# Performance work log

Measured on AMD Instinct MI355X. Metric: run time of the kernel, lower is better.

## Reference

```python
import jax, jax.numpy as jnp
import numpy as np

EPS = 1e-8  # torch F.cosine_similarity default eps


def setup_inputs() -> dict:
    key = jax.random.key(0)
    k1, k2 = jax.random.split(key)
    x = jax.random.normal(k1, (16384, 1024), dtype=jnp.float32)
    label = jax.random.randint(k2, (16384, 64), 0, 2).astype(jnp.int64)
    w = jnp.asarray(10.0, dtype=jnp.float32)  # nn.Parameter init_w
    b = jnp.asarray(-5.0, dtype=jnp.float32)  # nn.Parameter init_b
    return {"x": x, "label": label, "w": w, "b": b}


def reference(x, label, w, b):
    # Append the 'no-label' column for rows whose label vector is all zero.
    extra = (label.sum(axis=1) == 0).astype(label.dtype)[:, None]
    lab = jnp.concatenate([label, extra], axis=1).astype(x.dtype)  # [B, C]

    counts = lab.sum(axis=0)                  # [C] positives per centroid
    active = counts > 0                       # torch drops empty columns; we mask them

    # Centroids: mean of x over rows carrying each label (scatter-mean as GEMM).
    anchor = (lab.T @ x) / jnp.maximum(counts, 1.0)[:, None]   # [C, D]

    # Cosine similarity between every sample and every centroid.
    xn = jnp.maximum(jnp.linalg.norm(x, axis=1), EPS)          # [B]
    an = jnp.maximum(jnp.linalg.norm(anchor, axis=1), EPS)     # [C]
    cos = (x @ anchor.T) / (xn[:, None] * an[None, :])          # [B, C]

    logits = cos * w + b
    # Removing empty columns from softmax == setting their logits to -inf.
    logits = jnp.where(active[None, :], logits, -jnp.inf)
    logp = jax.nn.log_softmax(logits, axis=1)                   # [B, C]

    # Row expansion in torch duplicates sample i once per positive label j;
    # the logits row only depends on i, so CE over expanded rows is a
    # pair-weighted mean of -logp[i, j] over positive (i, j) pairs.
    n_pairs = lab.sum()
    nloss = -jnp.sum(jnp.where(lab > 0, logp, 0.0)) / n_pairs
    return nloss
```

## Files before the change

kernel.cpp:

```cpp
#include <hip/hip_runtime.h>
#include <hip/hip_bf16.h>
#include <stdint.h>

#define NROWS 16384
#define NDIM  1024
#define NLAB  64
#define NC    65
#define CPAD  80

typedef float float4v __attribute__((ext_vector_type(4)));
typedef short short8  __attribute__((ext_vector_type(8)));

static constexpr size_t SCALE_B = 0;
static constexpr size_t ACTB_B  = 320;
static constexpr size_t WSUM_B  = 400;
static constexpr size_t CNTF_B  = 448;
static constexpr size_t CNTP_B  = 1024;
static constexpr size_t MASK_B  = 83968;
static constexpr size_t XN2_B   = 215040;
static constexpr size_t LFRAG_B = 280576;
static constexpr size_t BFRAG_B = 2902016;
static constexpr size_t XAF_B   = 3065856;
static constexpr size_t XCOL_B  = 36620288;
static constexpr size_t PART_B  = 70174720;
static constexpr size_t SLAB    = (size_t)CPAD * NDIM * 4;

__device__ __forceinline__ unsigned short bf16u(float f) {
    __hip_bfloat16 h = __float2bfloat16(f);
    return __builtin_bit_cast(unsigned short, h);
}
__device__ __forceinline__ unsigned pk2(float a, float b) {
    return (unsigned)bf16u(a) | ((unsigned)bf16u(b) << 16);
}

__global__ __launch_bounds__(256) void k01_prep(const float* __restrict__ x,
                                                const int* __restrict__ label,
                                                unsigned short* __restrict__ xAfrag,
                                                unsigned short* __restrict__ xcol,
                                                float* __restrict__ xn2g,
                                                unsigned long long* __restrict__ masks,
                                                unsigned* __restrict__ cntpart,
                                                unsigned short* __restrict__ lfrag) {
    __shared__ unsigned short xt[16][1034];
    __shared__ unsigned cnt[NC];
    __shared__ unsigned long long smask[64];
    int t = threadIdx.x;
    if (blockIdx.x < 1024) {
        int rt = blockIdx.x;
        int r = t >> 4, cpos = t & 15;
        const float* src = x + ((size_t)rt * 16 + r) * NDIM + cpos * 4;
        float sq = 0.f;
#pragma unroll
        for (int i = 0; i < 16; ++i) {
            float4 f = *(const float4*)(src + i * 64);
            sq += f.x * f.x + f.y * f.y + f.z * f.z + f.w * f.w;
            *(uint2*)&xt[r][cpos * 4 + i * 64] = make_uint2(pk2(f.x, f.y), pk2(f.z, f.w));
        }
#pragma unroll
        for (int m = 1; m < 16; m <<= 1) sq += __shfl_xor(sq, m, 16);
        if (cpos == 0) xn2g[rt * 16 + r] = sq;
        __syncthreads();
        {
            int slot = t & 63, wv = t >> 6;
            int q = slot >> 4, col = slot & 15;
#pragma unroll
            for (int s = 0; s < 8; ++s) {
                int kb = s * 4 + wv;
                uint4 v = *(const uint4*)&xt[col][kb * 32 + q * 8];
                ((uint4*)xAfrag)[((size_t)rt * 32 + kb) * 64 + slot] = v;
            }
        }
#pragma unroll
        for (int s = 0; s < 8; ++s) {
            int dim = s * 128 + (t >> 1);
            int rh = (t & 1) * 8;
            unsigned short tmp[8];
#pragma unroll
            for (int j = 0; j < 8; ++j) tmp[j] = xt[rh + j][dim];
            uint4 v;
            v.x = (unsigned)tmp[0] | ((unsigned)tmp[1] << 16);
            v.y = (unsigned)tmp[2] | ((unsigned)tmp[3] << 16);
            v.z = (unsigned)tmp[4] | ((unsigned)tmp[5] << 16);
            v.w = (unsigned)tmp[6] | ((unsigned)tmp[7] << 16);
            ((uint4*)xcol)[(size_t)rt * 2048 + s * 256 + t] = v;
        }
        return;
    }
    int bid = blockIdx.x - 1024;
    if (t < NC) cnt[t] = 0;
    __syncthreads();
    int wave = t >> 6, lane = t & 63;
    int rowblock = bid * 64;
    unsigned creg = 0, zreg = 0;
#pragma unroll 4
    for (int p = 0; p < 16; ++p) {
        int row = rowblock + p * 4 + wave;
        int v = label[row * NLAB + lane];
        unsigned long long m = __ballot(v != 0);
        creg += (unsigned)((m >> lane) & 1ull);
        if (lane == 0) {
            masks[row] = m;
            smask[p * 4 + wave] = m;
            zreg += (m == 0ull) ? 1u : 0u;
        }
    }
    atomicAdd(&cnt[lane], creg);
    if (lane == 0 && zreg) atomicAdd(&cnt[64], zreg);
    __syncthreads();
    if (t < 80) cntpart[bid * 80 + t] = (t < NC) ? cnt[t] : 0u;
    for (int pid = t; pid < 640; pid += 256) {
        int rt2l = pid / 320, rem = pid % 320;
        int ct = rem >> 6, ln = rem & 63;
        int q = ln >> 4, col = ln & 15;
        int c = ct * 16 + col;
        int rbase = rt2l * 32 + q * 8;
        unsigned pk[4];
#pragma unroll
        for (int jp = 0; jp < 4; ++jp) {
            unsigned long long m0 = smask[rbase + jp * 2], m1 = smask[rbase + jp * 2 + 1];
            unsigned b0, b1;
            if (c < 64)       { b0 = (unsigned)((m0 >> c) & 1ull); b1 = (unsigned)((m1 >> c) & 1ull); }
            else if (c == 64) { b0 = (m0 == 0ull); b1 = (m1 == 0ull); }
            else              { b0 = 0u; b1 = 0u; }
            pk[jp] = (b0 ? 0x3F80u : 0u) | (b1 ? 0x3F800000u : 0u);
        }
        uint4 w = make_uint4(pk[0], pk[1], pk[2], pk[3]);
        ((uint4*)lfrag)[((size_t)(bid * 2 + rt2l) * 5 + ct) * 64 + ln] = w;
    }
}

__global__ __launch_bounds__(256) void k2_sums(const unsigned short* __restrict__ xcol,
                                               const unsigned short* __restrict__ lfrag,
                                               float* __restrict__ partial,
                                               int kslices) {
    int t = threadIdx.x, wave = t >> 6, lane = t & 63;
    int q = lane >> 4, col = lane & 15;
    int dgroup = blockIdx.x & 15, ks = blockIdx.x >> 4;
    int nkb = (NROWS / kslices) >> 5;
    int kb0 = ks * nkb;
    int d = dgroup * 64 + wave * 16 + col;
    const uint4* B = (const uint4*)xcol;
    const uint4* A = (const uint4*)lfrag;
    size_t bidx0 = (size_t)d * 2 + (q & 1);
    int qh = q >> 1;

    float4v acc[5];
#pragma unroll
    for (int ct = 0; ct < 5; ++ct) acc[ct] = (float4v){0.f, 0.f, 0.f, 0.f};

    uint4 b0 = B[(size_t)((kb0 + 0) * 2 + qh) * 2048 + bidx0];
    uint4 a0[5];
#pragma unroll
    for (int ct = 0; ct < 5; ++ct) a0[ct] = A[((size_t)(kb0 + 0) * 5 + ct) * 64 + lane];
    uint4 b1 = B[(size_t)((kb0 + 1) * 2 + qh) * 2048 + bidx0];
    uint4 a1[5];
#pragma unroll
    for (int ct = 0; ct < 5; ++ct) a1[ct] = A[((size_t)(kb0 + 1) * 5 + ct) * 64 + lane];

    for (int i = 0; i < nkb; i += 2) {
        int p2 = i + 2 < nkb ? kb0 + i + 2 : kb0 + i;
        int p3 = i + 3 < nkb ? kb0 + i + 3 : kb0 + i + 1;
        {
            short8 bf = __builtin_bit_cast(short8, b0);
#pragma unroll
            for (int ct = 0; ct < 5; ++ct) {
                short8 af = __builtin_bit_cast(short8, a0[ct]);
                acc[ct] = __builtin_amdgcn_mfma_f32_16x16x32_bf16(af, bf, acc[ct], 0, 0, 0);
            }
            b0 = B[(size_t)(p2 * 2 + qh) * 2048 + bidx0];
#pragma unroll
            for (int ct = 0; ct < 5; ++ct) a0[ct] = A[((size_t)p2 * 5 + ct) * 64 + lane];
        }
        {
            short8 bf = __builtin_bit_cast(short8, b1);
#pragma unroll
            for (int ct = 0; ct < 5; ++ct) {
                short8 af = __builtin_bit_cast(short8, a1[ct]);
                acc[ct] = __builtin_amdgcn_mfma_f32_16x16x32_bf16(af, bf, acc[ct], 0, 0, 0);
            }
            b1 = B[(size_t)(p3 * 2 + qh) * 2048 + bidx0];
#pragma unroll
            for (int ct = 0; ct < 5; ++ct) a1[ct] = A[((size_t)p3 * 5 + ct) * 64 + lane];
        }
    }
    float* pb = partial + (size_t)ks * CPAD * NDIM;
#pragma unroll
    for (int ct = 0; ct < 5; ++ct)
#pragma unroll
        for (int reg = 0; reg < 4; ++reg)
            pb[(size_t)(ct * 16 + q * 4 + reg) * NDIM + d] = acc[ct][reg];
}

__global__ __launch_bounds__(1024) void k2b_fuse(const float* __restrict__ wptr,
                                                 const unsigned* __restrict__ cntpart,
                                                 const float* __restrict__ partial,
                                                 int kslices,
                                                 unsigned short* __restrict__ bfrag,
                                                 float* __restrict__ scale,
                                                 unsigned char* __restrict__ actB,
                                                 unsigned* __restrict__ countsF,
                                                 float* __restrict__ wsum) {
    int c = blockIdx.x, t = threadIdx.x;
    __shared__ float red[16];
    __shared__ unsigned credu[4];
    __shared__ float bcast[2];
    if (c == 0 && t == 512) *wsum = 0.f;
    if (t < 256) {
        unsigned cv = cntpart[t * 80 + c];
#pragma unroll
        for (int m = 32; m >= 1; m >>= 1) cv += __shfl_xor(cv, m, 64);
        if ((t & 63) == 0) credu[t >> 6] = cv;
    }
    __syncthreads();
    unsigned cnt = credu[0] + credu[1] + credu[2] + credu[3];

    const float* p = partial + (size_t)c * NDIM + t;
    float s = 0.f;
#pragma unroll 8
    for (int sl = 0; sl < kslices; ++sl)
        s += p[(size_t)sl * CPAD * NDIM];
    float invc = 1.0f / (float)(cnt > 0u ? cnt : 1u);
    float a = s * invc;
    float ss = a * a;
#pragma unroll
    for (int m = 32; m >= 1; m >>= 1) ss += __shfl_xor(ss, m, 64);
    if ((t & 63) == 0) red[t >> 6] = ss;
    __syncthreads();
    if (t == 0) {
        float tot = 0.f;
#pragma unroll
        for (int j = 0; j < 16; ++j) tot += red[j];
        bcast[0] = fmaxf(sqrtf(tot), 1e-8f);
    }
    __syncthreads();
    float rinv = 1.0f / bcast[0];
    unsigned short h = bf16u(a * rinv);
    int ct = c >> 4, colc = c & 15;
    int kb = t >> 5, q = (t >> 3) & 3, j0 = t & 7;
    bfrag[((((size_t)ct * 32 + kb) * 64) + q * 16 + colc) * 8 + j0] = h;
    float hv = __bfloat162float(__builtin_bit_cast(__hip_bfloat16, h));
    float nb2 = hv * hv;
#pragma unroll
    for (int m = 32; m >= 1; m >>= 1) nb2 += __shfl_xor(nb2, m, 64);
    if ((t & 63) == 0) red[t >> 6] = nb2;
    __syncthreads();
    if (t == 0) {
        float n2 = 0.f;
#pragma unroll
        for (int j = 0; j < 16; ++j) n2 += red[j];
        scale[c] = (n2 > 0.f) ? (wptr[0] / sqrtf(n2)) : 0.f;
        actB[c] = (cnt > 0u) ? 1 : 0;
        countsF[c] = cnt;
    }
}

__global__ __launch_bounds__(256) void k3_loss(const unsigned short* __restrict__ xAfrag,
                                               const unsigned short* __restrict__ bfrag,
                                               const float* __restrict__ xn2g,
                                               const unsigned long long* __restrict__ masks,
                                               const unsigned char* __restrict__ actB,
                                               const float* __restrict__ scale,
                                               const float* __restrict__ bptr,
                                               float* __restrict__ wsum) {
    int t = threadIdx.x, wave = t >> 6, lane = t & 63;
    int q = lane >> 4, col = lane & 15;
    int rt = blockIdx.x * 4 + wave;
    int rowbase = rt * 16;
    const uint4* A = (const uint4*)xAfrag + (size_t)rt * 32 * 64 + lane;
    const uint4* Bp = (const uint4*)bfrag + lane;

    float4v acc[5];
#pragma unroll
    for (int ct = 0; ct < 5; ++ct) acc[ct] = (float4v){0.f, 0.f, 0.f, 0.f};

    uint4 a0 = A[0], a1 = A[64];
    uint4 b0[5], b1[5];
#pragma unroll
    for (int ct = 0; ct < 5; ++ct) b0[ct] = Bp[(size_t)(ct * 32 + 0) * 64];
#pragma unroll
    for (int ct = 0; ct < 5; ++ct) b1[ct] = Bp[(size_t)(ct * 32 + 1) * 64];

    for (int s = 0; s < 32; s += 2) {
        int p2 = s + 2 < 32 ? s + 2 : s;
        int p3 = s + 3 < 32 ? s + 3 : s + 1;
        {
            short8 af = __builtin_bit_cast(short8, a0);
#pragma unroll
            for (int ct = 0; ct < 5; ++ct) {
                short8 bf = __builtin_bit_cast(short8, b0[ct]);
                acc[ct] = __builtin_amdgcn_mfma_f32_16x16x32_bf16(af, bf, acc[ct], 0, 0, 0);
            }
            a0 = A[p2 * 64];
#pragma unroll
            for (int ct = 0; ct < 5; ++ct) b0[ct] = Bp[(size_t)(ct * 32 + p2) * 64];
        }
        {
            short8 af = __builtin_bit_cast(short8, a1);
#pragma unroll
            for (int ct = 0; ct < 5; ++ct) {
                short8 bf = __builtin_bit_cast(short8, b1[ct]);
                acc[ct] = __builtin_amdgcn_mfma_f32_16x16x32_bf16(af, bf, acc[ct], 0, 0, 0);
            }
            a1 = A[p3 * 64];
#pragma unroll
            for (int ct = 0; ct < 5; ++ct) b1[ct] = Bp[(size_t)(ct * 32 + p3) * 64];
        }
    }

    float bv = bptr[0];
    float sc[5]; unsigned char ab[5];
#pragma unroll
    for (int ct = 0; ct < 5; ++ct) { sc[ct] = scale[ct * 16 + col]; ab[ct] = actB[ct * 16 + col]; }

    float contrib = 0.f;
#pragma unroll
    for (int reg = 0; reg < 4; ++reg) {
        int rl = q * 4 + reg;
        int row = rowbase + rl;
        float inv = 1.0f / fmaxf(sqrtf(xn2g[row]), 1e-8f);
        unsigned long long mask = masks[row];
        float v[5]; float lmax = -1e30f;
#pragma unroll
        for (int ct = 0; ct < 5; ++ct) {
            float lg = acc[ct][reg] * sc[ct] * inv + bv;
            v[ct] = ab[ct] ? lg : -1e30f;
            lmax = fmaxf(lmax, v[ct]);
        }
#pragma unroll
        for (int m = 1; m < 16; m <<= 1) lmax = fmaxf(lmax, __shfl_xor(lmax, m, 16));
        float es = 0.f;
#pragma unroll
        for (int ct = 0; ct < 5; ++ct) es += expf(v[ct] - lmax);
#pragma unroll
        for (int m = 1; m < 16; m <<= 1) es += __shfl_xor(es, m, 16);
        float lse = lmax + logf(es);
        float ps = 0.f;
#pragma unroll
        for (int ct = 0; ct < 5; ++ct) {
            int c = ct * 16 + col;
            bool pos = (c < 64) ? (((mask >> c) & 1ull) != 0ull)
                                : ((c == 64) ? (mask == 0ull) : false);
            ps += pos ? v[ct] : 0.f;
        }
#pragma unroll
        for (int m = 1; m < 16; m <<= 1) ps += __shfl_xor(ps, m, 16);
        float npos = mask ? (float)__popcll(mask) : 1.0f;
        float crow = ps - npos * lse;
        if (col == 0) contrib += crow;
    }
#pragma unroll
    for (int m = 1; m < 64; m <<= 1) contrib += __shfl_xor(contrib, m, 64);
    if (lane == 0) atomicAdd(wsum, contrib);
}

__global__ void k4_final(const unsigned* __restrict__ countsF,
                         const float* __restrict__ wsum,
                         float* __restrict__ out) {
    if (threadIdx.x == 0 && blockIdx.x == 0) {
        float np = 0.f;
        for (int c = 0; c < NC; ++c) np += (float)countsF[c];
        out[0] = -wsum[0] / np;
    }
}

extern "C" void kernel_launch(void* const* d_in, const int* in_sizes, int n_in,
                              void* d_out, int out_size, void* d_ws, size_t ws_size,
                              hipStream_t stream) {
    (void)in_sizes; (void)n_in; (void)out_size;
    const float* x = (const float*)d_in[0];
    const int* label = (const int*)d_in[1];
    const float* w = (const float*)d_in[2];
    const float* b = (const float*)d_in[3];

    char* ws = (char*)d_ws;
    float* scale = (float*)(ws + SCALE_B);
    unsigned char* actB = (unsigned char*)(ws + ACTB_B);
    float* wsum = (float*)(ws + WSUM_B);
    unsigned* countsF = (unsigned*)(ws + CNTF_B);
    unsigned* cntpart = (unsigned*)(ws + CNTP_B);
    unsigned long long* masks = (unsigned long long*)(ws + MASK_B);
    float* xn2g = (float*)(ws + XN2_B);
    unsigned short* lfrag = (unsigned short*)(ws + LFRAG_B);
    unsigned short* bfrag = (unsigned short*)(ws + BFRAG_B);
    unsigned short* xAfrag = (unsigned short*)(ws + XAF_B);
    unsigned short* xcol = (unsigned short*)(ws + XCOL_B);
    float* partial = (float*)(ws + PART_B);

    int kslices = 32;
    while (kslices > 8 && PART_B + (size_t)kslices * SLAB > ws_size) kslices >>= 1;

    hipLaunchKernelGGL(k01_prep, dim3(1024 + 256), dim3(256), 0, stream,
                       x, label, xAfrag, xcol, xn2g, masks, cntpart, lfrag);
    hipLaunchKernelGGL(k2_sums, dim3(16 * kslices), dim3(256), 0, stream,
                       xcol, lfrag, partial, kslices);
    hipLaunchKernelGGL(k2b_fuse, dim3(CPAD), dim3(1024), 0, stream,
                       w, cntpart, partial, kslices, bfrag, scale, actB, countsF, wsum);
    hipLaunchKernelGGL(k3_loss, dim3(NROWS / 64), dim3(256), 0, stream,
                       xAfrag, bfrag, xn2g, masks, actB, scale, b, wsum);
    hipLaunchKernelGGL(k4_final, dim3(1), dim3(64), 0, stream, countsF, wsum, (float*)d_out);
}
```

Measured before the change: 163.3 us.

## Restructure prep transpose, split centroid reduction, and split-K the loss GEMM

In the prep kernel, all x loads are issued before any use, and the xcol transpose now reads shared memory as 128-bit vectors and interleaves them with byte-permute into a new xcol layout. The k2_sums indexing is updated to match that layout. The centroid reduction is split into a wide kernel over 320 blocks that sums the k-slices and partial norms, plus a small finalize kernel, and k-slices go from 32 to 64. The loss GEMM now assigns one 16-row tile per block with split-K across its four waves, reduced through shared memory. These changes aim to add parallelism and memory-level concurrency, at the cost of one extra launch, more partial traffic and shared-memory reductions.

```diff
diff --git a/kernel.cpp b/kernel.cpp
--- a/kernel.cpp
+++ b/kernel.cpp
@@ -24,6 +24,8 @@
 static constexpr size_t XCOL_B  = 36620288;
 static constexpr size_t PART_B  = 70174720;
 static constexpr size_t SLAB    = (size_t)CPAD * NDIM * 4;
+static constexpr size_t ANCH_SZ = (size_t)CPAD * NDIM * 4;
+static constexpr size_t NRM_SZ  = (size_t)CPAD * 4 * 4;
 
 __device__ __forceinline__ unsigned short bf16u(float f) {
     __hip_bfloat16 h = __float2bfloat16(f);
@@ -41,20 +43,22 @@
                                                 unsigned long long* __restrict__ masks,
                                                 unsigned* __restrict__ cntpart,
                                                 unsigned short* __restrict__ lfrag) {
-    __shared__ unsigned short xt[16][1034];
+    __shared__ unsigned short xt[16][1040];
     __shared__ unsigned cnt[NC];
     __shared__ unsigned long long smask[64];
     int t = threadIdx.x;
     if (blockIdx.x < 1024) {
         int rt = blockIdx.x;
         int r = t >> 4, cpos = t & 15;
-        const float* src = x + ((size_t)rt * 16 + r) * NDIM + cpos * 4;
+        const float4* src = (const float4*)(x + ((size_t)rt * 16 + r) * NDIM) + cpos;
+        float4 f[16];
+#pragma unroll
+        for (int i = 0; i < 16; ++i) f[i] = src[i * 16];
         float sq = 0.f;
 #pragma unroll
         for (int i = 0; i < 16; ++i) {
-            float4 f = *(const float4*)(src + i * 64);
-            sq += f.x * f.x + f.y * f.y + f.z * f.z + f.w * f.w;
-            *(uint2*)&xt[r][cpos * 4 + i * 64] = make_uint2(pk2(f.x, f.y), pk2(f.z, f.w));
+            sq += f[i].x * f[i].x + f[i].y * f[i].y + f[i].z * f[i].z + f[i].w * f[i].w;
+            *(uint2*)&xt[r][cpos * 4 + i * 64] = make_uint2(pk2(f[i].x, f[i].y), pk2(f[i].z, f[i].w));
         }
 #pragma unroll
         for (int m = 1; m < 16; m <<= 1) sq += __shfl_xor(sq, m, 16);
@@ -70,19 +74,25 @@
                 ((uint4*)xAfrag)[((size_t)rt * 32 + kb) * 64 + slot] = v;
             }
         }
-#pragma unroll
-        for (int s = 0; s < 8; ++s) {
-            int dim = s * 128 + (t >> 1);
-            int rh = (t & 1) * 8;
-            unsigned short tmp[8];
-#pragma unroll
-            for (int j = 0; j < 8; ++j) tmp[j] = xt[rh + j][dim];
-            uint4 v;
-            v.x = (unsigned)tmp[0] | ((unsigned)tmp[1] << 16);
-            v.y = (unsigned)tmp[2] | ((unsigned)tmp[3] << 16);
-            v.z = (unsigned)tmp[4] | ((unsigned)tmp[5] << 16);
-            v.w = (unsigned)tmp[6] | ((unsigned)tmp[7] << 16);
-            ((uint4*)xcol)[(size_t)rt * 2048 + s * 256 + t] = v;
+        {
+            int rh8 = (t & 1) * 8, dg = t >> 1;
+            uint4 R[8];
+#pragma unroll
+            for (int j = 0; j < 8; ++j) R[j] = *(const uint4*)&xt[rh8 + j][dg * 8];
+            uint4* dst = (uint4*)xcol + (size_t)rt * 2048 + t * 8;
+#pragma unroll
+            for (int p = 0; p < 4; ++p) {
+                unsigned lo[4], hi[4];
+#pragma unroll
+                for (int jj = 0; jj < 4; ++jj) {
+                    unsigned A0 = ((const unsigned*)&R[2 * jj])[p];
+                    unsigned B0 = ((const unsigned*)&R[2 * jj + 1])[p];
+                    lo[jj] = __builtin_amdgcn_perm(B0, A0, 0x05040100u);
+                    hi[jj] = __builtin_amdgcn_perm(B0, A0, 0x07060302u);
+                }
+                dst[2 * p]     = make_uint4(lo[0], lo[1], lo[2], lo[3]);
+                dst[2 * p + 1] = make_uint4(hi[0], hi[1], hi[2], hi[3]);
+            }
         }
         return;
     }
@@ -141,7 +151,7 @@
     int d = dgroup * 64 + wave * 16 + col;
     const uint4* B = (const uint4*)xcol;
     const uint4* A = (const uint4*)lfrag;
-    size_t bidx0 = (size_t)d * 2 + (q & 1);
+    size_t bidx0 = (size_t)((d >> 3) * 16 + (q & 1) * 8 + (d & 7));
     int qh = q >> 1;
 
     float4v acc[5];
@@ -191,19 +201,39 @@
             pb[(size_t)(ct * 16 + q * 4 + reg) * NDIM + d] = acc[ct][reg];
 }
 
-__global__ __launch_bounds__(1024) void k2b_fuse(const float* __restrict__ wptr,
-                                                 const unsigned* __restrict__ cntpart,
-                                                 const float* __restrict__ partial,
-                                                 int kslices,
-                                                 unsigned short* __restrict__ bfrag,
-                                                 float* __restrict__ scale,
-                                                 unsigned char* __restrict__ actB,
-                                                 unsigned* __restrict__ countsF,
-                                                 float* __restrict__ wsum) {
+__global__ __launch_bounds__(256) void k2bA(const float* __restrict__ partial,
+                                            int kslices,
+                                            float* __restrict__ anchor_raw,
+                                            float* __restrict__ norm2part) {
+    __shared__ float red[4];
+    int c = blockIdx.x >> 2, dq = blockIdx.x & 3, t = threadIdx.x;
+    int d = dq * 256 + t;
+    const float* p = partial + (size_t)c * NDIM + d;
+    float s = 0.f;
+#pragma unroll 8
+    for (int sl = 0; sl < kslices; ++sl) s += p[(size_t)sl * CPAD * NDIM];
+    anchor_raw[(size_t)c * NDIM + d] = s;
+    float ss = s * s;
+#pragma unroll
+    for (int m = 32; m >= 1; m >>= 1) ss += __shfl_xor(ss, m, 64);
+    if ((t & 63) == 0) red[t >> 6] = ss;
+    __syncthreads();
+    if (t == 0) norm2part[blockIdx.x] = red[0] + red[1] + red[2] + red[3];
+}
+
+__global__ __launch_bounds__(1024) void k2bB(const float* __restrict__ wptr,
+                                             const unsigned* __restrict__ cntpart,
+                                             const float* __restrict__ anchor_raw,
+                                             const float* __restrict__ norm2part,
+                                             unsigned short* __restrict__ bfrag,
+                                             float* __restrict__ scale,
+                                             unsigned char* __restrict__ actB,
+                                             unsigned* __restrict__ countsF,
+                                             float* __restrict__ wsum) {
     int c = blockIdx.x, t = threadIdx.x;
     __shared__ float red[16];
     __shared__ unsigned credu[4];
-    __shared__ float bcast[2];
+    __shared__ float bcast[1];
     if (c == 0 && t == 512) *wsum = 0.f;
     if (t < 256) {
         unsigned cv = cntpart[t * 80 + c];
@@ -211,30 +241,15 @@
         for (int m = 32; m >= 1; m >>= 1) cv += __shfl_xor(cv, m, 64);
         if ((t & 63) == 0) credu[t >> 6] = cv;
     }
+    if (t == 0)
+        bcast[0] = sqrtf(norm2part[c * 4] + norm2part[c * 4 + 1] +
+                         norm2part[c * 4 + 2] + norm2part[c * 4 + 3]);
     __syncthreads();
     unsigned cnt = credu[0] + credu[1] + credu[2] + credu[3];
-
-    const float* p = partial + (size_t)c * NDIM + t;
-    float s = 0.f;
-#pragma unroll 8
-    for (int sl = 0; sl < kslices; ++sl)
-        s += p[(size_t)sl * CPAD * NDIM];
     float invc = 1.0f / (float)(cnt > 0u ? cnt : 1u);
-    float a = s * invc;
-    float ss = a * a;
-#pragma unroll
-    for (int m = 32; m >= 1; m >>= 1) ss += __shfl_xor(ss, m, 64);
-    if ((t & 63) == 0) red[t >> 6] = ss;
-    __syncthreads();
-    if (t == 0) {
-        float tot = 0.f;
-#pragma unroll
-        for (int j = 0; j < 16; ++j) tot += red[j];
-        bcast[0] = fmaxf(sqrtf(tot), 1e-8f);
-    }
-    __syncthreads();
-    float rinv = 1.0f / bcast[0];
-    unsigned short h = bf16u(a * rinv);
+    float a = anchor_raw[(size_t)c * NDIM + t] * invc;
+    float an = fmaxf(bcast[0] * invc, 1e-8f);
+    unsigned short h = bf16u(a / an);
     int ct = c >> 4, colc = c & 15;
     int kb = t >> 5, q = (t >> 3) & 3, j0 = t & 7;
     bfrag[((((size_t)ct * 32 + kb) * 64) + q * 16 + colc) * 8 + j0] = h;
@@ -262,27 +277,29 @@
                                                const float* __restrict__ scale,
                                                const float* __restrict__ bptr,
                                                float* __restrict__ wsum) {
+    __shared__ float redsm[3][64][21];
     int t = threadIdx.x, wave = t >> 6, lane = t & 63;
     int q = lane >> 4, col = lane & 15;
-    int rt = blockIdx.x * 4 + wave;
+    int rt = blockIdx.x;
     int rowbase = rt * 16;
     const uint4* A = (const uint4*)xAfrag + (size_t)rt * 32 * 64 + lane;
     const uint4* Bp = (const uint4*)bfrag + lane;
+    int kb0 = wave * 8;
 
     float4v acc[5];
 #pragma unroll
     for (int ct = 0; ct < 5; ++ct) acc[ct] = (float4v){0.f, 0.f, 0.f, 0.f};
 
-    uint4 a0 = A[0], a1 = A[64];
+    uint4 a0 = A[(size_t)(kb0 + 0) * 64], a1 = A[(size_t)(kb0 + 1) * 64];
     uint4 b0[5], b1[5];
 #pragma unroll
-    for (int ct = 0; ct < 5; ++ct) b0[ct] = Bp[(size_t)(ct * 32 + 0) * 64];
-#pragma unroll
-    for (int ct = 0; ct < 5; ++ct) b1[ct] = Bp[(size_t)(ct * 32 + 1) * 64];
-
-    for (int s = 0; s < 32; s += 2) {
-        int p2 = s + 2 < 32 ? s + 2 : s;
-        int p3 = s + 3 < 32 ? s + 3 : s + 1;
+    for (int ct = 0; ct < 5; ++ct) b0[ct] = Bp[(size_t)(ct * 32 + kb0 + 0) * 64];
+#pragma unroll
+    for (int ct = 0; ct < 5; ++ct) b1[ct] = Bp[(size_t)(ct * 32 + kb0 + 1) * 64];
+
+    for (int s = 0; s < 8; s += 2) {
+        int p2 = s + 2 < 8 ? kb0 + s + 2 : kb0 + s;
+        int p3 = s + 3 < 8 ? kb0 + s + 3 : kb0 + s + 1;
         {
             short8 af = __builtin_bit_cast(short8, a0);
 #pragma unroll
@@ -290,7 +307,7 @@
                 short8 bf = __builtin_bit_cast(short8, b0[ct]);
                 acc[ct] = __builtin_amdgcn_mfma_f32_16x16x32_bf16(af, bf, acc[ct], 0, 0, 0);
             }
-            a0 = A[p2 * 64];
+            a0 = A[(size_t)p2 * 64];
 #pragma unroll
             for (int ct = 0; ct < 5; ++ct) b0[ct] = Bp[(size_t)(ct * 32 + p2) * 64];
         }
@@ -301,11 +318,28 @@
                 short8 bf = __builtin_bit_cast(short8, b1[ct]);
                 acc[ct] = __builtin_amdgcn_mfma_f32_16x16x32_bf16(af, bf, acc[ct], 0, 0, 0);
             }
-            a1 = A[p3 * 64];
+            a1 = A[(size_t)p3 * 64];
 #pragma unroll
             for (int ct = 0; ct < 5; ++ct) b1[ct] = Bp[(size_t)(ct * 32 + p3) * 64];
         }
     }
+
+    if (wave) {
+#pragma unroll
+        for (int ct = 0; ct < 5; ++ct)
+#pragma unroll
+            for (int reg = 0; reg < 4; ++reg)
+                redsm[wave - 1][lane][ct * 4 + reg] = acc[ct][reg];
+    }
+    __syncthreads();
+    if (wave != 0) return;
+#pragma unroll
+    for (int w = 0; w < 3; ++w)
+#pragma unroll
+        for (int ct = 0; ct < 5; ++ct)
+#pragma unroll
+            for (int reg = 0; reg < 4; ++reg)
+                acc[ct][reg] += redsm[w][lane][ct * 4 + reg];
 
     float bv = bptr[0];
     float sc[5]; unsigned char ab[5];
@@ -386,16 +420,21 @@
     unsigned short* xcol = (unsigned short*)(ws + XCOL_B);
     float* partial = (float*)(ws + PART_B);
 
-    int kslices = 32;
-    while (kslices > 8 && PART_B + (size_t)kslices * SLAB > ws_size) kslices >>= 1;
+    int kslices = 64;
+    while (kslices > 8 && PART_B + (size_t)kslices * SLAB + ANCH_SZ + NRM_SZ > ws_size)
+        kslices >>= 1;
+    float* anchor_raw = (float*)(ws + PART_B + (size_t)kslices * SLAB);
+    float* norm2part = anchor_raw + CPAD * NDIM;
 
     hipLaunchKernelGGL(k01_prep, dim3(1024 + 256), dim3(256), 0, stream,
                        x, label, xAfrag, xcol, xn2g, masks, cntpart, lfrag);
     hipLaunchKernelGGL(k2_sums, dim3(16 * kslices), dim3(256), 0, stream,
                        xcol, lfrag, partial, kslices);
-    hipLaunchKernelGGL(k2b_fuse, dim3(CPAD), dim3(1024), 0, stream,
-                       w, cntpart, partial, kslices, bfrag, scale, actB, countsF, wsum);
-    hipLaunchKernelGGL(k3_loss, dim3(NROWS / 64), dim3(256), 0, stream,
+    hipLaunchKernelGGL(k2bA, dim3(CPAD * 4), dim3(256), 0, stream,
+                       partial, kslices, anchor_raw, norm2part);
+    hipLaunchKernelGGL(k2bB, dim3(CPAD), dim3(1024), 0, stream,
+                       w, cntpart, anchor_raw, norm2part, bfrag, scale, actB, countsF, wsum);
+    hipLaunchKernelGGL(k3_loss, dim3(NROWS / 16), dim3(256), 0, stream,
                        xAfrag, bfrag, xn2g, masks, actB, scale, b, wsum);
     hipLaunchKernelGGL(k4_final, dim3(1), dim3(64), 0, stream, countsF, wsum, (float*)d_out);
 }
```

Measured after the change: 172.2 us. 1.05x slower.
